# Kernel tuning notes

Measured on AMD Instinct MI355X. Metric: run time of the kernel, lower is better.

The kernel has to match this reference:

```python
import jax, jax.numpy as jnp
import numpy as np
from jax import lax

B, C, XH, XW, KH, KW = 32, 128, 96, 96, 3, 3
BN_EPS = 1e-5


def setup_inputs() -> dict:
    key = jax.random.key(0)
    k1, k2, k3 = jax.random.split(key, 3)
    x = jax.random.normal(k1, (B, C, XH, XW), dtype=jnp.float32)
    k = jax.random.normal(k2, (B, C, KH, KW), dtype=jnp.float32)
    pw_weight = jax.random.normal(k3, (C, C), dtype=jnp.float32) * (1.0 / np.sqrt(C))
    bn_gamma = jnp.ones((C,), dtype=jnp.float32)
    bn_beta = jnp.zeros((C,), dtype=jnp.float32)
    bn_mean = jnp.zeros((C,), dtype=jnp.float32)
    bn_var = jnp.ones((C,), dtype=jnp.float32)
    return {"x": x, "k": k, "pw_weight": pw_weight, "bn_gamma": bn_gamma,
            "bn_beta": bn_beta, "bn_mean": bn_mean, "bn_var": bn_var}


def _depthwise_one(xi, ki):
    # xi: [C, XH, XW], ki: [C, KH, KW] -> per-sample depthwise conv, padding=KH//2
    pad = KH // 2
    out = lax.conv_general_dilated(
        xi[None],                 # [1, C, XH, XW]
        ki[:, None],              # [C, 1, KH, KW]  (OIHW with groups=C)
        window_strides=(1, 1),
        padding=((pad, pad), (pad, pad)),
        feature_group_count=C,
        dimension_numbers=("NCHW", "OIHW", "NCHW"),
    )
    return out[0]


def reference(x, k, pw_weight, bn_gamma, bn_beta, bn_mean, bn_var):
    # Per-sample dynamic depthwise conv, batched via vmap (replaces the Python loop)
    x_new = jax.vmap(_depthwise_one)(x, k)          # [B, C, XH, XW]
    # 1x1 pointwise conv (no bias)
    y = jnp.einsum("bchw,oc->bohw", x_new, pw_weight)
    # BatchNorm (inference form with running stats) + ReLU
    inv = bn_gamma * lax.rsqrt(bn_var + BN_EPS)
    y = y * inv[None, :, None, None] + (bn_beta - bn_mean * inv)[None, :, None, None]
    return jax.nn.relu(y)
```

## Files before the change

kernel.cpp:

```cpp
#include <hip/hip_runtime.h>
#include <hip/hip_bf16.h>

#define BB 32
#define CC 128
#define HH 96
#define WW 96
#define BN_EPS 1e-5f

typedef __attribute__((ext_vector_type(8))) short bf16x8_t;
typedef __attribute__((ext_vector_type(4))) float f32x4_t;
typedef __attribute__((ext_vector_type(4), aligned(4))) float f32x4u_t;
typedef __attribute__((ext_vector_type(2))) unsigned int u32x2_t;
typedef __attribute__((ext_vector_type(4))) unsigned int u32x4_t;

__global__ __launch_bounds__(256)
void prep_kernel(const float* __restrict__ pw,
                 const float* __restrict__ g, const float* __restrict__ b,
                 const float* __restrict__ m, const float* __restrict__ v,
                 unsigned short* __restrict__ wper,
                 float* __restrict__ inv, float* __restrict__ bias)
{
    int t = blockIdx.x * 256 + threadIdx.x;
    if (t < CC * CC) {
        int o = t >> 7, cidx = t & 127;
        int kc = cidx >> 5, r = cidx & 31, gg = r >> 3, j = r & 7;
        int c = kc * 32 + gg * 4 + (j & 3) + 16 * (j >> 2);
        __hip_bfloat16 h = __float2bfloat16(pw[o * CC + c]);
        wper[o * CC + cidx] = *reinterpret_cast<unsigned short*>(&h);
    }
    if (t < CC) {
        float iv = g[t] * rsqrtf(v[t] + BN_EPS);
        inv[t] = iv;
        bias[t] = b[t] - m[t] * iv;
    }
}

__global__ __launch_bounds__(256, 6)
void dw_kernel(const float* __restrict__ x, const float* __restrict__ kk,
               unsigned short* __restrict__ xn)
{
    __shared__ float tile[18 * 96];
    const int tid = threadIdx.x;

    const unsigned wg  = blockIdx.x;
    const unsigned bid = (wg & 7u) * 3072u + (wg >> 3);
    const int slab = bid % 6u;
    const int cs   = (bid / 6u) % 128u;
    const int b    = bid / 768u;
    const int h0   = slab * 16;

    const int kc = cs >> 5, rr = cs & 31, gg = rr >> 3, jj = rr & 7;
    const int c = kc * 32 + gg * 4 + (jj & 3) + 16 * (jj >> 2);

    const float* plane = x + (size_t)(b * CC + c) * (HH * WW);

    const float* kp = kk + (size_t)(b * CC + c) * 9;
    const float kw0 = kp[0], kw1 = kp[1], kw2 = kp[2];
    const float kw3 = kp[3], kw4 = kp[4], kw5 = kp[5];
    const float kw6 = kp[6], kw7 = kp[7], kw8 = kp[8];

    #pragma unroll
    for (int it = 0; it < 2; ++it) {
        const int s = tid + it * 256;
        if (s < 432) {
            const int row  = s / 24;
            const int col4 = (s % 24) * 4;
            const int hh   = h0 - 1 + row;
            f32x4_t val = (f32x4_t){0.f, 0.f, 0.f, 0.f};
            if (hh >= 0 && hh < HH)
                val = *(const f32x4_t*)(plane + (size_t)hh * WW + col4);
            *(f32x4_t*)&tile[row * 96 + col4] = val;
        }
    }
    __syncthreads();

    const int r  = tid >> 4;
    const int cc = (tid & 15) * 6;

    float v[3][8];
    #pragma unroll
    for (int dr = 0; dr < 3; ++dr) {
        const float* trow = &tile[(r + dr) * 96];
        const float lv = trow[cc == 0 ? 0 : cc - 1];
        v[dr][0] = (cc == 0) ? 0.f : lv;
        #pragma unroll
        for (int i = 0; i < 6; ++i) v[dr][1 + i] = trow[cc + i];
        const float rv = trow[cc == 90 ? 95 : cc + 6];
        v[dr][7] = (cc == 90) ? 0.f : rv;
    }

    unsigned pk[3];
    #pragma unroll
    for (int pr = 0; pr < 3; ++pr) {
        float s0, s1;
        const int j0 = 2 * pr;
        s0 = v[0][j0] * kw0;                   const int j1 = j0 + 1;
        s0 = fmaf(v[0][j0 + 1], kw1, s0);
        s0 = fmaf(v[0][j0 + 2], kw2, s0);
        s0 = fmaf(v[1][j0],     kw3, s0);
        s0 = fmaf(v[1][j0 + 1], kw4, s0);
        s0 = fmaf(v[1][j0 + 2], kw5, s0);
        s0 = fmaf(v[2][j0],     kw6, s0);
        s0 = fmaf(v[2][j0 + 1], kw7, s0);
        s0 = fmaf(v[2][j0 + 2], kw8, s0);
        s1 = v[0][j1] * kw0;
        s1 = fmaf(v[0][j1 + 1], kw1, s1);
        s1 = fmaf(v[0][j1 + 2], kw2, s1);
        s1 = fmaf(v[1][j1],     kw3, s1);
        s1 = fmaf(v[1][j1 + 1], kw4, s1);
        s1 = fmaf(v[1][j1 + 2], kw5, s1);
        s1 = fmaf(v[2][j1],     kw6, s1);
        s1 = fmaf(v[2][j1 + 1], kw7, s1);
        s1 = fmaf(v[2][j1 + 2], kw8, s1);
        __hip_bfloat16 h0b = __float2bfloat16(s0);
        __hip_bfloat16 h1b = __float2bfloat16(s1);
        pk[pr] = (unsigned)*reinterpret_cast<unsigned short*>(&h0b)
               | ((unsigned)*reinterpret_cast<unsigned short*>(&h1b) << 16);
    }

    unsigned short* dst = xn + (size_t)(b * CC + cs) * (HH * WW)
                             + (size_t)(h0 + r) * WW + cc;
    *reinterpret_cast<unsigned*>(dst)     = pk[0];
    *reinterpret_cast<unsigned*>(dst + 2) = pk[1];
    *reinterpret_cast<unsigned*>(dst + 4) = pk[2];
}

__global__ __launch_bounds__(256, 3)
void pw_kernel(const unsigned short* __restrict__ xn,
               const unsigned short* __restrict__ wper,
               const float* __restrict__ invp, const float* __restrict__ biasp,
               float* __restrict__ out)
{
    __shared__ __align__(16) unsigned char xnb[128 * 256];
    const int tid = threadIdx.x;

    const unsigned wg  = blockIdx.x;
    const unsigned nid = (wg & 7u) * 96u + (wg >> 3);
    const int tw  = nid % 6u;
    const int thg = (nid / 6u) % 4u;
    const int b   = nid / 24u;
    const int w0  = tw * 16;

    const int lane   = tid & 63;
    const int wv     = tid >> 6;
    const int lo     = lane & 15;
    const int hi     = lane >> 4;
    const int o_base = wv * 32;

    bf16x8_t wfrag[2][4];
    #pragma unroll
    for (int t2 = 0; t2 < 2; ++t2)
        #pragma unroll
        for (int kc = 0; kc < 4; ++kc)
            wfrag[t2][kc] = *reinterpret_cast<const bf16x8_t*>(
                wper + (size_t)(o_base + t2 * 16 + lo) * CC + kc * 32 + hi * 8);

    float iv2[2], bs2[2];
    #pragma unroll
    for (int t2 = 0; t2 < 2; ++t2) {
        iv2[t2] = invp[o_base + t2 * 16 + lo];
        bs2[t2] = biasp[o_base + t2 * 16 + lo];
    }

    const int cs4 = tid >> 3;
    const int py  = tid & 7;
    const unsigned short* src_base =
        xn + (size_t)(b * CC + cs4 * 4) * (HH * WW) + (size_t)py * WW + w0;

    unsigned dLA[4][4], dRA[4][4], dLB[4][4], dRB[4][4];

    auto LOADREGS = [&](int t, unsigned (*dL)[4], unsigned (*dR)[4]) {
        const unsigned short* s0 = src_base + (size_t)((thg * 3 + t) * 8) * WW;
        #pragma unroll
        for (int q = 0; q < 4; ++q) {
            const unsigned short* src = s0 + (size_t)q * (HH * WW);
            u32x4_t L = *(const u32x4_t*)src;
            u32x4_t R = *(const u32x4_t*)(src + 8);
            dL[q][0]=L.x; dL[q][1]=L.y; dL[q][2]=L.z; dL[q][3]=L.w;
            dR[q][0]=R.x; dR[q][1]=R.y; dR[q][2]=R.z; dR[q][3]=R.w;
        }
    };

    auto WRITE_LDS = [&](unsigned (*dL)[4], unsigned (*dR)[4]) {
        #pragma unroll
        for (int o8 = 0; o8 < 2; ++o8) {
            #pragma unroll
            for (int j = 0; j < 4; ++j) {
                const unsigned d0 = o8 ? dR[0][j] : dL[0][j];
                const unsigned d1 = o8 ? dR[1][j] : dL[1][j];
                const unsigned d2 = o8 ? dR[2][j] : dL[2][j];
                const unsigned d3 = o8 ? dR[3][j] : dL[3][j];
                u32x2_t we, wo;
                we.x = __builtin_amdgcn_perm(d1, d0, 0x05040100u);
                we.y = __builtin_amdgcn_perm(d3, d2, 0x05040100u);
                wo.x = __builtin_amdgcn_perm(d1, d0, 0x07060302u);
                wo.y = __builtin_amdgcn_perm(d3, d2, 0x07060302u);
                const int pe = py * 16 + o8 * 8 + 2 * j;
                const int po = pe + 1;
                *reinterpret_cast<u32x2_t*>(&xnb[(unsigned)pe * 256 +
                    (((unsigned)cs4 * 8) ^ (((unsigned)pe & 7u) << 4))]) = we;
                *reinterpret_cast<u32x2_t*>(&xnb[(unsigned)po * 256 +
                    (((unsigned)cs4 * 8) ^ (((unsigned)po & 7u) << 4))]) = wo;
            }
        }
    };

    auto COMPUTE = [&](int t) {
        const int h0 = (thg * 3 + t) * 8;
        f32x4_t acc[8][2];
        #pragma unroll
        for (int pt = 0; pt < 8; ++pt) {
            acc[pt][0] = (f32x4_t){0.f, 0.f, 0.f, 0.f};
            acc[pt][1] = (f32x4_t){0.f, 0.f, 0.f, 0.f};
        }
        #pragma unroll
        for (int pt = 0; pt < 8; ++pt) {
            const unsigned rowbase = (unsigned)(pt * 16 + lo) * 256;
            const unsigned sw = (unsigned)((lo & 7) << 4);
            #pragma unroll
            for (int kc = 0; kc < 4; ++kc) {
                bf16x8_t xfrag = *reinterpret_cast<const bf16x8_t*>(
                    &xnb[rowbase + (((unsigned)(kc * 64 + hi * 16)) ^ sw)]);
                acc[pt][0] = __builtin_amdgcn_mfma_f32_16x16x32_bf16(
                    xfrag, wfrag[0][kc], acc[pt][0], 0, 0, 0);
                acc[pt][1] = __builtin_amdgcn_mfma_f32_16x16x32_bf16(
                    xfrag, wfrag[1][kc], acc[pt][1], 0, 0, 0);
            }
        }
        #pragma unroll
        for (int pt = 0; pt < 8; ++pt) {
            const int hrow = h0 + pt;
            #pragma unroll
            for (int t2 = 0; t2 < 2; ++t2) {
                const int o = o_base + t2 * 16 + lo;
                f32x4_t vv;
                #pragma unroll
                for (int rix = 0; rix < 4; ++rix)
                    vv[rix] = fmaxf(fmaf(acc[pt][t2][rix], iv2[t2], bs2[t2]), 0.f);
                __builtin_nontemporal_store(vv, reinterpret_cast<f32x4_t*>(
                    out + ((size_t)(b * CC + o) * HH + hrow) * WW + w0 + hi * 4));
            }
        }
    };

    LOADREGS(0, dLA, dRA);
    WRITE_LDS(dLA, dRA);
    LOADREGS(1, dLB, dRB);
    __syncthreads();
    COMPUTE(0);
    __syncthreads();
    WRITE_LDS(dLB, dRB);
    LOADREGS(2, dLA, dRA);
    __syncthreads();
    COMPUTE(1);
    __syncthreads();
    WRITE_LDS(dLA, dRA);
    __syncthreads();
    COMPUTE(2);
}

__global__ __launch_bounds__(256, 3)
void fused_main(const float* __restrict__ x, const float* __restrict__ kk,
                const unsigned short* __restrict__ wper,
                const float* __restrict__ invp, const float* __restrict__ biasp,
                float* __restrict__ out)
{
    __shared__ __align__(16) unsigned char xnb[128 * 256];
    const int tid = threadIdx.x;
    const unsigned wg  = blockIdx.x;
    const unsigned nid = (wg & 7u) * 288u + (wg >> 3);
    const int bx = nid % 6u;
    const int by = (nid / 6u) % 12u;
    const int bb = nid / 72u;
    const int w0 = bx * 16;
    const int h0 = by * 8;
    {
        const int wq = tid & 3;
        const int cp = tid >> 2;
        const int s  = cp << 1;
        const int kc = s >> 5, rr = s & 31, gg = rr >> 3, jj = rr & 7;
        const int cA = kc * 32 + gg * 4 + (jj & 3) + 16 * (jj >> 2);
        const int gw = w0 + wq * 4;
        const bool l_edge = (gw == 0);
        const bool r_edge = (gw + 4 >= WW);
        const float* planeA = x + (size_t)(bb * CC + cA) * (HH * WW);
        float kwA[9], kwB[9];
        {
            const float* kp = kk + (size_t)(bb * CC + cA) * 9;
            f32x4u_t q0 = *(const f32x4u_t*)(kp + 0);
            f32x4u_t q1 = *(const f32x4u_t*)(kp + 4);
            f32x4u_t q2 = *(const f32x4u_t*)(kp + 8);
            f32x4u_t q3 = *(const f32x4u_t*)(kp + 12);
            float     e16 = kp[16], e17 = kp[17];
            kwA[0]=q0.x; kwA[1]=q0.y; kwA[2]=q0.z; kwA[3]=q0.w;
            kwA[4]=q1.x; kwA[5]=q1.y; kwA[6]=q1.z; kwA[7]=q1.w;
            kwA[8]=q2.x;
            kwB[0]=q2.y; kwB[1]=q2.z; kwB[2]=q2.w;
            kwB[3]=q3.x; kwB[4]=q3.y; kwB[5]=q3.z; kwB[6]=q3.w;
            kwB[7]=e16;  kwB[8]=e17;
        }
        float xd[2][10][6];
        #pragma unroll
        for (int q = 0; q < 2; ++q) {
            const float* plane = planeA + q * (HH * WW);
            #pragma unroll
            for (int r = 0; r < 10; ++r) {
                const int row = h0 - 1 + r;
                const bool valid = (row >= 0) && (row < HH);
                const int rrow = row < 0 ? 0 : (row >= HH ? HH - 1 : row);
                const float* rp = plane + rrow * WW + gw;
                f32x4_t M = *(const f32x4_t*)rp;
                float vl = rp[l_edge ? 0 : -1];
                float vr = rp[r_edge ? 3 : 4];
                xd[q][r][0] = (valid && !l_edge) ? vl : 0.f;
                xd[q][r][1] = valid ? M.x : 0.f;
                xd[q][r][2] = valid ? M.y : 0.f;
                xd[q][r][3] = valid ? M.z : 0.f;
                xd[q][r][4] = valid ? M.w : 0.f;
                xd[q][r][5] = (valid && !r_edge) ? vr : 0.f;
            }
        }
        #pragma unroll
        for (int py = 0; py < 8; ++py) {
            #pragma unroll
            for (int i = 0; i < 4; ++i) {
                float sA = 0.f, sB = 0.f;
                #pragma unroll
                for (int t = 0; t < 3; ++t) {
                    sA = fmaf(xd[0][py + 0][i + t], kwA[t],     sA);
                    sA = fmaf(xd[0][py + 1][i + t], kwA[3 + t], sA);
                    sA = fmaf(xd[0][py + 2][i + t], kwA[6 + t], sA);
                    sB = fmaf(xd[1][py + 0][i + t], kwB[t],     sB);
                    sB = fmaf(xd[1][py + 1][i + t], kwB[3 + t], sB);
                    sB = fmaf(xd[1][py + 2][i + t], kwB[6 + t], sB);
                }
                __hip_bfloat16 hA = __float2bfloat16(sA);
                __hip_bfloat16 hB = __float2bfloat16(sB);
                unsigned pk = (unsigned)*reinterpret_cast<unsigned short*>(&hA)
                            | ((unsigned)*reinterpret_cast<unsigned short*>(&hB) << 16);
                const int p = py * 16 + wq * 4 + i;
                const unsigned boff = ((unsigned)(cp << 2)) ^ (((unsigned)p & 7u) << 4);
                *reinterpret_cast<unsigned*>(&xnb[(unsigned)p * 256 + boff]) = pk;
            }
        }
    }
    __syncthreads();
    {
        const int lane   = tid & 63;
        const int wv     = tid >> 6;
        const int lo     = lane & 15;
        const int hi     = lane >> 4;
        const int o_base = wv * 32;
        bf16x8_t afrag[2][4];
        #pragma unroll
        for (int t2 = 0; t2 < 2; ++t2)
            #pragma unroll
            for (int kc = 0; kc < 4; ++kc)
                afrag[t2][kc] = *reinterpret_cast<const bf16x8_t*>(
                    wper + (size_t)(o_base + t2 * 16 + lo) * CC + kc * 32 + hi * 8);
        f32x4_t acc[8][2];
        #pragma unroll
        for (int pt = 0; pt < 8; ++pt) {
            acc[pt][0] = (f32x4_t){0.f, 0.f, 0.f, 0.f};
            acc[pt][1] = (f32x4_t){0.f, 0.f, 0.f, 0.f};
        }
        #pragma unroll
        for (int pt = 0; pt < 8; ++pt) {
            const unsigned rowbase = (unsigned)(pt * 16 + lo) * 256;
            const unsigned sw = (unsigned)((lo & 7) << 4);
            #pragma unroll
            for (int kc = 0; kc < 4; ++kc) {
                bf16x8_t bfrag = *reinterpret_cast<const bf16x8_t*>(
                    &xnb[rowbase + (((unsigned)(kc * 64 + hi * 16)) ^ sw)]);
                acc[pt][0] = __builtin_amdgcn_mfma_f32_16x16x32_bf16(
                    afrag[0][kc], bfrag, acc[pt][0], 0, 0, 0);
                acc[pt][1] = __builtin_amdgcn_mfma_f32_16x16x32_bf16(
                    afrag[1][kc], bfrag, acc[pt][1], 0, 0, 0);
            }
        }
        float iv[2][4], bs[2][4];
        #pragma unroll
        for (int t2 = 0; t2 < 2; ++t2)
            #pragma unroll
            for (int r = 0; r < 4; ++r) {
                const int o = o_base + t2 * 16 + hi * 4 + r;
                iv[t2][r] = invp[o];
                bs[t2][r] = biasp[o];
            }
        #pragma unroll
        for (int pt = 0; pt < 8; ++pt) {
            const int hrow = h0 + pt;
            #pragma unroll
            for (int t2 = 0; t2 < 2; ++t2) {
                #pragma unroll
                for (int r = 0; r < 4; ++r) {
                    const int o = o_base + t2 * 16 + hi * 4 + r;
                    float val = fmaf(acc[pt][t2][r], iv[t2][r], bs[t2][r]);
                    val = fmaxf(val, 0.f);
                    out[((size_t)(bb * CC + o) * HH + hrow) * WW + w0 + lo] = val;
                }
            }
        }
    }
}

extern "C" void kernel_launch(void* const* d_in, const int* in_sizes, int n_in,
                              void* d_out, int out_size, void* d_ws, size_t ws_size,
                              hipStream_t stream) {
    const float* x   = (const float*)d_in[0];
    const float* kk  = (const float*)d_in[1];
    const float* pwt = (const float*)d_in[2];
    const float* g   = (const float*)d_in[3];
    const float* b   = (const float*)d_in[4];
    const float* m   = (const float*)d_in[5];
    const float* v   = (const float*)d_in[6];
    float* out = (float*)d_out;

    unsigned short* wper = (unsigned short*)d_ws;
    float* inv  = (float*)((char*)d_ws + 32768);
    float* bias = (float*)((char*)d_ws + 32768 + 512);
    unsigned short* xn = (unsigned short*)((char*)d_ws + 36864);
    const size_t need = 36864 + (size_t)BB * CC * HH * WW * 2;

    prep_kernel<<<64, 256, 0, stream>>>(pwt, g, b, m, v, wper, inv, bias);
    if (ws_size >= need) {
        dw_kernel<<<dim3(24576), 256, 0, stream>>>(x, kk, xn);
        pw_kernel<<<dim3(768), 256, 0, stream>>>(xn, wper, inv, bias, out);
    } else {
        fused_main<<<dim3(2304), 256, 0, stream>>>(x, kk, wper, inv, bias, out);
    }
}
```

Before: 94.49 us.

## Make depthwise kernel persistent per plane with double-buffered slab prefetch

Each depthwise workgroup now processes a whole (batch, channel) plane across six 16-row slabs instead of one slab, cutting the grid from 24576 to 4096 workgroups. Global loads for slab t+2 are held in registers while slab t is computed, and the LDS tile is double-buffered with a 97-float row pitch. This amortizes kernel-weight loads and halo rereads and overlaps memory latency with compute. The cost is more registers per thread, scalar LDS writes instead of vector writes, and fewer workgroups to hide latency.

```diff
diff --git a/kernel.cpp b/kernel.cpp
--- a/kernel.cpp
+++ b/kernel.cpp
@@ -39,90 +39,114 @@
 void dw_kernel(const float* __restrict__ x, const float* __restrict__ kk,
                unsigned short* __restrict__ xn)
 {
-    __shared__ float tile[18 * 96];
+    __shared__ float tile[2][18 * 97];
     const int tid = threadIdx.x;
 
     const unsigned wg  = blockIdx.x;
-    const unsigned bid = (wg & 7u) * 3072u + (wg >> 3);
-    const int slab = bid % 6u;
-    const int cs   = (bid / 6u) % 128u;
-    const int b    = bid / 768u;
-    const int h0   = slab * 16;
+    const unsigned bid = (wg & 7u) * 512u + (wg >> 3);
+    const int cs = bid & 127;
+    const int b  = bid >> 7;
 
     const int kc = cs >> 5, rr = cs & 31, gg = rr >> 3, jj = rr & 7;
     const int c = kc * 32 + gg * 4 + (jj & 3) + 16 * (jj >> 2);
 
     const float* plane = x + (size_t)(b * CC + c) * (HH * WW);
+    unsigned short* xplane = xn + (size_t)(b * CC + cs) * (HH * WW);
 
     const float* kp = kk + (size_t)(b * CC + c) * 9;
     const float kw0 = kp[0], kw1 = kp[1], kw2 = kp[2];
     const float kw3 = kp[3], kw4 = kp[4], kw5 = kp[5];
     const float kw6 = kp[6], kw7 = kp[7], kw8 = kp[8];
 
-    #pragma unroll
-    for (int it = 0; it < 2; ++it) {
-        const int s = tid + it * 256;
-        if (s < 432) {
-            const int row  = s / 24;
-            const int col4 = (s % 24) * 4;
-            const int hh   = h0 - 1 + row;
-            f32x4_t val = (f32x4_t){0.f, 0.f, 0.f, 0.f};
-            if (hh >= 0 && hh < HH)
-                val = *(const f32x4_t*)(plane + (size_t)hh * WW + col4);
-            *(f32x4_t*)&tile[row * 96 + col4] = val;
-        }
-    }
-    __syncthreads();
+    const int sA = tid;
+    const int sB = tid + 256;
+    const int rowA = sA / 24, colA = (sA % 24) * 4;
+    const int rowB = sB / 24, colB = (sB % 24) * 4;
+
+    f32x4_t gA[2], gB[2];
+
+    auto LOADG = [&](int t, f32x4_t* gr) {
+        const int hhA = t * 16 - 1 + rowA;
+        gr[0] = (f32x4_t){0.f, 0.f, 0.f, 0.f};
+        if (hhA >= 0 && hhA < HH)
+            gr[0] = *(const f32x4_t*)(plane + (size_t)hhA * WW + colA);
+        gr[1] = (f32x4_t){0.f, 0.f, 0.f, 0.f};
+        if (sB < 432) {
+            const int hhB = t * 16 - 1 + rowB;
+            if (hhB >= 0 && hhB < HH)
+                gr[1] = *(const f32x4_t*)(plane + (size_t)hhB * WW + colB);
+        }
+    };
+
+    auto DSWRITE = [&](int bufi, f32x4_t* gr) {
+        float* d0 = &tile[bufi][rowA * 97 + colA];
+        d0[0] = gr[0].x; d0[1] = gr[0].y; d0[2] = gr[0].z; d0[3] = gr[0].w;
+        if (sB < 432) {
+            float* d1 = &tile[bufi][rowB * 97 + colB];
+            d1[0] = gr[1].x; d1[1] = gr[1].y; d1[2] = gr[1].z; d1[3] = gr[1].w;
+        }
+    };
 
     const int r  = tid >> 4;
     const int cc = (tid & 15) * 6;
 
-    float v[3][8];
+    auto COMPUTE = [&](int bufi, int t) {
+        float v[3][8];
+        #pragma unroll
+        for (int dr = 0; dr < 3; ++dr) {
+            const float* trow = &tile[bufi][(r + dr) * 97];
+            const float lv = trow[cc == 0 ? 0 : cc - 1];
+            v[dr][0] = (cc == 0) ? 0.f : lv;
+            #pragma unroll
+            for (int i = 0; i < 6; ++i) v[dr][1 + i] = trow[cc + i];
+            const float rv = trow[cc == 90 ? 95 : cc + 6];
+            v[dr][7] = (cc == 90) ? 0.f : rv;
+        }
+        unsigned pk[3];
+        #pragma unroll
+        for (int pr = 0; pr < 3; ++pr) {
+            const int j0 = 2 * pr, j1 = j0 + 1;
+            float s0 = v[0][j0] * kw0;
+            s0 = fmaf(v[0][j0 + 1], kw1, s0);
+            s0 = fmaf(v[0][j0 + 2], kw2, s0);
+            s0 = fmaf(v[1][j0],     kw3, s0);
+            s0 = fmaf(v[1][j0 + 1], kw4, s0);
+            s0 = fmaf(v[1][j0 + 2], kw5, s0);
+            s0 = fmaf(v[2][j0],     kw6, s0);
+            s0 = fmaf(v[2][j0 + 1], kw7, s0);
+            s0 = fmaf(v[2][j0 + 2], kw8, s0);
+            float s1 = v[0][j1] * kw0;
+            s1 = fmaf(v[0][j1 + 1], kw1, s1);
+            s1 = fmaf(v[0][j1 + 2], kw2, s1);
+            s1 = fmaf(v[1][j1],     kw3, s1);
+            s1 = fmaf(v[1][j1 + 1], kw4, s1);
+            s1 = fmaf(v[1][j1 + 2], kw5, s1);
+            s1 = fmaf(v[2][j1],     kw6, s1);
+            s1 = fmaf(v[2][j1 + 1], kw7, s1);
+            s1 = fmaf(v[2][j1 + 2], kw8, s1);
+            __hip_bfloat16 h0b = __float2bfloat16(s0);
+            __hip_bfloat16 h1b = __float2bfloat16(s1);
+            pk[pr] = (unsigned)*reinterpret_cast<unsigned short*>(&h0b)
+                   | ((unsigned)*reinterpret_cast<unsigned short*>(&h1b) << 16);
+        }
+        unsigned short* dst = xplane + (size_t)(t * 16 + r) * WW + cc;
+        *reinterpret_cast<unsigned*>(dst)     = pk[0];
+        *reinterpret_cast<unsigned*>(dst + 2) = pk[1];
+        *reinterpret_cast<unsigned*>(dst + 4) = pk[2];
+    };
+
+    LOADG(0, gA);
+    DSWRITE(0, gA);
+    LOADG(1, gB);
+    __syncthreads();
+
     #pragma unroll
-    for (int dr = 0; dr < 3; ++dr) {
-        const float* trow = &tile[(r + dr) * 96];
-        const float lv = trow[cc == 0 ? 0 : cc - 1];
-        v[dr][0] = (cc == 0) ? 0.f : lv;
-        #pragma unroll
-        for (int i = 0; i < 6; ++i) v[dr][1 + i] = trow[cc + i];
-        const float rv = trow[cc == 90 ? 95 : cc + 6];
-        v[dr][7] = (cc == 90) ? 0.f : rv;
-    }
-
-    unsigned pk[3];
-    #pragma unroll
-    for (int pr = 0; pr < 3; ++pr) {
-        float s0, s1;
-        const int j0 = 2 * pr;
-        s0 = v[0][j0] * kw0;                   const int j1 = j0 + 1;
-        s0 = fmaf(v[0][j0 + 1], kw1, s0);
-        s0 = fmaf(v[0][j0 + 2], kw2, s0);
-        s0 = fmaf(v[1][j0],     kw3, s0);
-        s0 = fmaf(v[1][j0 + 1], kw4, s0);
-        s0 = fmaf(v[1][j0 + 2], kw5, s0);
-        s0 = fmaf(v[2][j0],     kw6, s0);
-        s0 = fmaf(v[2][j0 + 1], kw7, s0);
-        s0 = fmaf(v[2][j0 + 2], kw8, s0);
-        s1 = v[0][j1] * kw0;
-        s1 = fmaf(v[0][j1 + 1], kw1, s1);
-        s1 = fmaf(v[0][j1 + 2], kw2, s1);
-        s1 = fmaf(v[1][j1],     kw3, s1);
-        s1 = fmaf(v[1][j1 + 1], kw4, s1);
-        s1 = fmaf(v[1][j1 + 2], kw5, s1);
-        s1 = fmaf(v[2][j1],     kw6, s1);
-        s1 = fmaf(v[2][j1 + 1], kw7, s1);
-        s1 = fmaf(v[2][j1 + 2], kw8, s1);
-        __hip_bfloat16 h0b = __float2bfloat16(s0);
-        __hip_bfloat16 h1b = __float2bfloat16(s1);
-        pk[pr] = (unsigned)*reinterpret_cast<unsigned short*>(&h0b)
-               | ((unsigned)*reinterpret_cast<unsigned short*>(&h1b) << 16);
-    }
-
-    unsigned short* dst = xn + (size_t)(b * CC + cs) * (HH * WW)
-                             + (size_t)(h0 + r) * WW + cc;
-    *reinterpret_cast<unsigned*>(dst)     = pk[0];
-    *reinterpret_cast<unsigned*>(dst + 2) = pk[1];
-    *reinterpret_cast<unsigned*>(dst + 4) = pk[2];
+    for (int t = 0; t < 6; ++t) {
+        if (t + 2 < 6) LOADG(t + 2, (t & 1) ? gB : gA);
+        COMPUTE(t & 1, t);
+        if (t + 1 < 6) DSWRITE((t + 1) & 1, (t & 1) ? gA : gB);
+        __syncthreads();
+    }
 }
 
 __global__ __launch_bounds__(256, 3)
@@ -424,7 +448,7 @@
 
     prep_kernel<<<64, 256, 0, stream>>>(pwt, g, b, m, v, wper, inv, bias);
     if (ws_size >= need) {
-        dw_kernel<<<dim3(24576), 256, 0, stream>>>(x, kk, xn);
+        dw_kernel<<<dim3(4096), 256, 0, stream>>>(x, kk, xn);
         pw_kernel<<<dim3(768), 256, 0, stream>>>(xn, wper, inv, bias, out);
     } else {
         fused_main<<<dim3(2304), 256, 0, stream>>>(x, kk, wper, inv, bias, out);
```

Measured after the change: 95.32 us. About the same (+0.9%).
